# Kernel optimization log

Hardware: AMD Instinct MI355X
Metric: run time of the kernel (lower is better)

## Reference

```python
import jax, jax.numpy as jnp
import numpy as np

T, B, H, NH = 1024, 4, 1024, 16
D = H // NH


def setup_inputs() -> dict:
    key = jax.random.key(0)
    ks = jax.random.split(key, 8)
    s = 0.02
    return {
        "x": jax.random.normal(ks[0], (T, B, H), jnp.float32),
        "pos": jax.random.normal(ks[1], (2 * T - 1, 1, H), jnp.float32),
        "attn_mask": jnp.zeros((T, T), jnp.bool_),
        "ln_w": jnp.ones((H,), jnp.float32),
        "ln_b": jnp.zeros((H,), jnp.float32),
        "in_proj_w": jax.random.normal(ks[2], (3 * H, H), jnp.float32) * s,
        "in_proj_b": jnp.zeros((3 * H,), jnp.float32),
        "pos_proj_w": jax.random.normal(ks[3], (H, H), jnp.float32) * s,
        "r_w_bias": jax.random.normal(ks[4], (NH, D), jnp.float32) * s,
        "r_r_bias": jax.random.normal(ks[5], (NH, D), jnp.float32) * s,
        "out_proj_w": jax.random.normal(ks[6], (H, H), jnp.float32) * s,
        "out_proj_b": jnp.zeros((H,), jnp.float32),
    }


def _layer_norm(x, w, b, eps=1e-5):
    m = jnp.mean(x, axis=-1, keepdims=True)
    v = jnp.var(x, axis=-1, keepdims=True)
    return (x - m) * jax.lax.rsqrt(v + eps) * w + b


def _rel_shift(x):
    # x: [qlen, 2*qlen-1, B, NH] -> Transformer-XL relative shift
    q = x.shape[0]
    zero_pad = jnp.zeros((q, 1) + x.shape[2:], x.dtype)
    xp = jnp.concatenate([zero_pad, x], axis=1)            # [q, 2q, B, NH]
    xp = xp.reshape((x.shape[1] + 1, q) + x.shape[2:])     # [2q, q, B, NH]
    return xp[1:].reshape(x.shape)                         # [q, 2q-1, B, NH]


def reference(x, pos, attn_mask, ln_w, ln_b, in_proj_w, in_proj_b,
              pos_proj_w, r_w_bias, r_r_bias, out_proj_w, out_proj_b):
    # pre-norm
    qn = _layer_norm(x, ln_w, ln_b)                        # [T,B,H]
    # fused qkv projection
    qkv = qn @ in_proj_w.T + in_proj_b                     # [T,B,3H]
    q, k, v = jnp.split(qkv, 3, axis=-1)
    q = q.reshape(T, B, NH, D)
    k = k.reshape(T, B, NH, D)
    v = v.reshape(T, B, NH, D)
    # relative position keys (bias-free projection)
    r = (pos[:, 0] @ pos_proj_w.T).reshape(2 * T - 1, NH, D)
    # content term (AC) and position term (BD), Transformer-XL style
    AC = jnp.einsum('ibnd,jbnd->ijbn', q + r_w_bias, k)    # [T,T,B,NH]
    BD = jnp.einsum('ibnd,jnd->ijbn', q + r_r_bias, r)     # [T,2T-1,B,NH]
    BD = _rel_shift(BD)[:, :T]                             # [T,T,B,NH]
    scale = 1.0 / np.sqrt(D).astype(np.float32)
    score = (AC + BD) * scale
    score = jnp.where(attn_mask[:, :, None, None], -jnp.inf, score)
    p = jax.nn.softmax(score, axis=1)                      # coverage
    out = jnp.einsum('ijbn,jbnd->ibnd', p, v).reshape(T, B, H)
    o = out @ out_proj_w.T + out_proj_b                    # residual dropout = identity (eval)
    return o
```

## Files before the change

kernel.cpp:

```cpp
#include <hip/hip_runtime.h>
#include <hip/hip_bf16.h>
#include <math.h>

#define T_DIM 1024
#define B_DIM 4
#define H_DIM 1024
#define NHEAD 16
#define DHEAD 64
#define NROWS (T_DIM * B_DIM)
#define LPOS  (2 * T_DIM - 1)
#define QS    (3 * H_DIM)

typedef __attribute__((ext_vector_type(8))) short bfrag;
typedef __attribute__((ext_vector_type(4))) short sh4;
typedef __attribute__((ext_vector_type(4))) float facc;

static __device__ __forceinline__ short f2bf(float f) {
    return __builtin_bit_cast(short, __float2bfloat16(f));
}
static __device__ __forceinline__ float bf2f(short s) {
    unsigned u = ((unsigned)(unsigned short)s) << 16;
    return __builtin_bit_cast(float, u);
}

#define GLD16(g, l) __builtin_amdgcn_global_load_lds( \
    (const __attribute__((address_space(1))) void*)(g), \
    (__attribute__((address_space(3))) void*)(l), 16, 0, 0)

__global__ __launch_bounds__(256) void prep_kernel(
    const float* __restrict__ x, const float* __restrict__ lnw,
    const float* __restrict__ lnb, short* __restrict__ qn,
    const float* __restrict__ s0, short* __restrict__ d0, int c0,
    const float* __restrict__ s1, short* __restrict__ d1, int c1,
    const float* __restrict__ s2, short* __restrict__ d2, int c2,
    const float* __restrict__ s3, short* __restrict__ d3, int c3) {
    __shared__ float red0[4], red1[4];
    const int bid = blockIdx.x;
    const int tid = threadIdx.x;
    if (bid < NROWS) {
        const float* xr = x + (size_t)bid * H_DIM;
        short* yr = qn + (size_t)bid * H_DIM;
        float4 v = reinterpret_cast<const float4*>(xr)[tid];
        float s  = v.x + v.y + v.z + v.w;
        float sq = v.x * v.x + v.y * v.y + v.z * v.z + v.w * v.w;
        #pragma unroll
        for (int m = 32; m; m >>= 1) {
            s  += __shfl_xor(s, m);
            sq += __shfl_xor(sq, m);
        }
        int wave = tid >> 6, lane = tid & 63;
        if (lane == 0) { red0[wave] = s; red1[wave] = sq; }
        __syncthreads();
        float tot   = red0[0] + red0[1] + red0[2] + red0[3];
        float totsq = red1[0] + red1[1] + red1[2] + red1[3];
        float mean = tot * (1.0f / H_DIM);
        float var  = totsq * (1.0f / H_DIM) - mean * mean;
        float rstd = rsqrtf(var + 1e-5f);
        float4 wv = reinterpret_cast<const float4*>(lnw)[tid];
        float4 bv = reinterpret_cast<const float4*>(lnb)[tid];
        sh4 o;
        o[0] = f2bf((v.x - mean) * rstd * wv.x + bv.x);
        o[1] = f2bf((v.y - mean) * rstd * wv.y + bv.y);
        o[2] = f2bf((v.z - mean) * rstd * wv.z + bv.z);
        o[3] = f2bf((v.w - mean) * rstd * wv.w + bv.w);
        reinterpret_cast<sh4*>(yr)[tid] = o;
    } else {
        int i = (bid - NROWS) * 256 + tid;
        const float* s; short* d; int off;
        if      (i < c0)                { s = s0; d = d0; off = i; }
        else if (i < c0 + c1)           { s = s1; d = d1; off = i - c0; }
        else if (i < c0 + c1 + c2)      { s = s2; d = d2; off = i - c0 - c1; }
        else if (i < c0 + c1 + c2 + c3) { s = s3; d = d3; off = i - c0 - c1 - c2; }
        else return;
        const float* sp = s + (size_t)off * 8;
        float4 a = *(const float4*)(sp);
        float4 b = *(const float4*)(sp + 4);
        bfrag f;
        f[0] = f2bf(a.x); f[1] = f2bf(a.y); f[2] = f2bf(a.z); f[3] = f2bf(a.w);
        f[4] = f2bf(b.x); f[5] = f2bf(b.y); f[6] = f2bf(b.z); f[7] = f2bf(b.w);
        *(bfrag*)(d + (size_t)off * 8) = f;
    }
}

template<int MODE>
static __device__ __forceinline__ void gemm_body(
    const short* __restrict__ A, const short* __restrict__ B,
    const float* __restrict__ bias, void* __restrict__ Cv,
    int M, int N, int K, int gx, int nblk, int bid,
    short (*As)[64], short (*Bs)[64]) {
    const int tid = threadIdx.x;
    const int w4 = tid >> 6, l = tid & 63;
    const int lc = l & 15, lg = l >> 4;
    const int wr = w4 >> 1, wc = w4 & 1;

    const int cpx = nblk >> 3;
    const int nl = (bid & 7) * cpx + (bid >> 3);
    const int row0 = (nl / gx) * 128, col0 = (nl % gx) * 128;

    const int srow = l >> 3;
    const int schunk = ((l & 7) ^ srow) * 8;
    const int Mm1 = M - 1;

    facc acc[4][4];
    #pragma unroll
    for (int i = 0; i < 4; ++i)
        #pragma unroll
        for (int j = 0; j < 4; ++j) acc[i][j] = (facc){0.f, 0.f, 0.f, 0.f};

    for (int k0 = 0; k0 < K; k0 += 64) {
        #pragma unroll
        for (int p = 0; p < 4; ++p) {
            int rA = p * 32 + w4 * 8 + srow;
            int ga = row0 + rA; if (ga > Mm1) ga = Mm1;
            GLD16(A + (size_t)ga * K + k0 + schunk,
                  (char*)As + p * 4096 + w4 * 1024);
            GLD16(B + (size_t)(col0 + rA) * K + k0 + schunk,
                  (char*)Bs + p * 4096 + w4 * 1024);
        }
        __syncthreads();

        bfrag af[4][2], bfr[4][2];
        #pragma unroll
        for (int fr = 0; fr < 4; ++fr) {
            const int ra = wr * 64 + fr * 16 + lc;
            #pragma unroll
            for (int ks = 0; ks < 2; ++ks)
                af[fr][ks] = *(const bfrag*)&As[ra][(((ks * 4 + lg) ^ (ra & 7)) << 3)];
        }
        #pragma unroll
        for (int fc = 0; fc < 4; ++fc) {
            const int rb = wc * 64 + fc * 16 + lc;
            #pragma unroll
            for (int ks = 0; ks < 2; ++ks)
                bfr[fc][ks] = *(const bfrag*)&Bs[rb][(((ks * 4 + lg) ^ (rb & 7)) << 3)];
        }
        #pragma unroll
        for (int fr = 0; fr < 4; ++fr)
            #pragma unroll
            for (int fc = 0; fc < 4; ++fc)
                #pragma unroll
                for (int ks = 0; ks < 2; ++ks)
                    acc[fr][fc] = __builtin_amdgcn_mfma_f32_16x16x32_bf16(
                        af[fr][ks], bfr[fc][ks], acc[fr][fc], 0, 0, 0);
        __syncthreads();
    }

    #pragma unroll
    for (int fc = 0; fc < 4; ++fc) {
        const int gc = col0 + wc * 64 + fc * 16 + lc;
        const float bv = bias ? bias[gc] : 0.f;
        #pragma unroll
        for (int fr = 0; fr < 4; ++fr) {
            #pragma unroll
            for (int rg = 0; rg < 4; ++rg) {
                const int gr = row0 + wr * 64 + fr * 16 + lg * 4 + rg;
                if (gr < M) {
                    float o = acc[fr][fc][rg] + bv;
                    if constexpr (MODE == 0) ((float*)Cv)[(size_t)gr * N + gc] = o;
                    else                     ((short*)Cv)[(size_t)gr * N + gc] = f2bf(o);
                }
            }
        }
    }
}

__global__ __launch_bounds__(256) void gemm_dual(
    const short* __restrict__ A0, const short* __restrict__ B0,
    const float* __restrict__ bias0, short* __restrict__ C0,
    const short* __restrict__ A1, const short* __restrict__ B1,
    short* __restrict__ C1) {
    __shared__ short As[128][64];
    __shared__ short Bs[128][64];
    const int bid = blockIdx.x;
    if (bid < 768)
        gemm_body<1>(A0, B0, bias0, C0, NROWS, QS, H_DIM, QS / 128, 768, bid, As, Bs);
    else
        gemm_body<1>(A1, B1, nullptr, C1, LPOS, H_DIM, H_DIM, H_DIM / 128, 128, bid - 768, As, Bs);
}

__global__ __launch_bounds__(256) void gemm_f32out(
    const short* __restrict__ A, const short* __restrict__ B,
    const float* __restrict__ bias, float* __restrict__ C) {
    __shared__ short As[128][64];
    __shared__ short Bs[128][64];
    gemm_body<0>(A, B, bias, C, NROWS, H_DIM, H_DIM, H_DIM / 128, 256, blockIdx.x, As, Bs);
}

__global__ __launch_bounds__(256) void vtrans_kernel(const short* __restrict__ qkv,
                                                     short* __restrict__ vT) {
    __shared__ short T[64][72];
    const int tt = blockIdx.x, hh = blockIdx.y, b = blockIdx.z;
    const int tid = threadIdx.x;
    const int w = tid >> 6, lane = tid & 63;

    const int tg = tt * 64 + lane;
    const short* src = qkv + (size_t)(tg * B_DIM + b) * QS + 2 * H_DIM + hh * 64 + w * 16;
    bfrag v0 = *(const bfrag*)(src);
    bfrag v1 = *(const bfrag*)(src + 8);
    #pragma unroll
    for (int e = 0; e < 8; ++e) T[w * 16 + e][lane] = v0[e];
    #pragma unroll
    for (int e = 0; e < 8; ++e) T[w * 16 + 8 + e][lane] = v1[e];
    __syncthreads();

    const int hd = tid >> 2, tc = tid & 3;
    bfrag o0 = *(const bfrag*)&T[hd][tc * 16];
    bfrag o1 = *(const bfrag*)&T[hd][tc * 16 + 8];
    short* dst = vT + (((size_t)(b * H_DIM + hh * 64 + hd)) << 10) + tt * 64 + tc * 16;
    *(bfrag*)(dst) = o0;
    *(bfrag*)(dst + 8) = o1;
}

__global__ __launch_bounds__(512, 4) void attn_mfma(const short* __restrict__ qkv,
                                                    const short* __restrict__ r,
                                                    const short* __restrict__ vt,
                                                    const float* __restrict__ rwb,
                                                    const float* __restrict__ rrb,
                                                    short* __restrict__ out) {
    __shared__ short Ks[64][64];
    __shared__ short Vt[64][64];
    __shared__ short Rs[192][64];
    __shared__ short BDPs[8][16][84];

    const int d_   = blockIdx.x;
    const int slot = d_ >> 3, xcd = d_ & 7;
    const int bn   = xcd + 8 * (slot >> 3);
    const int i0   = (slot & 7) * 128;
    const int b    = bn >> 4;
    const int n    = bn & 15;

    const int tid = threadIdx.x;
    const int w   = tid >> 6;
    const int l   = tid & 63;
    const int lg  = l >> 4;
    const int lc  = l & 15;
    const int hoff = n * DHEAD;

    const int srow8 = l >> 3;
    const int sc8   = ((l & 7) ^ srow8) * 8;

    bfrag qw[2], qr[2];
    {
        const int row = i0 + 16 * w + lc;
        const short* qrow = qkv + (size_t)(row * B_DIM + b) * QS + hoff;
        #pragma unroll
        for (int ks = 0; ks < 2; ++ks) {
            const int d0 = ks * 32 + lg * 8;
            bfrag qv = *(const bfrag*)(qrow + d0);
            float4 wa = *(const float4*)(rwb + hoff + d0);
            float4 wb = *(const float4*)(rwb + hoff + d0 + 4);
            float4 ra = *(const float4*)(rrb + hoff + d0);
            float4 rb = *(const float4*)(rrb + hoff + d0 + 4);
            const float sc = 0.125f * 1.44269504f;
            float wf[8] = {wa.x, wa.y, wa.z, wa.w, wb.x, wb.y, wb.z, wb.w};
            float rf[8] = {ra.x, ra.y, ra.z, ra.w, rb.x, rb.y, rb.z, rb.w};
            bfrag fw, fr;
            #pragma unroll
            for (int e = 0; e < 8; ++e) {
                float qf = bf2f(qv[e]);
                fw[e] = f2bf((qf + wf[e]) * sc);
                fr[e] = f2bf((qf + rf[e]) * sc);
            }
            qw[ks] = fw; qr[ks] = fr;
        }
    }

    facc ofr[4];
    #pragma unroll
    for (int d = 0; d < 4; ++d) ofr[d] = (facc){0.f, 0.f, 0.f, 0.f};
    float lrow[4] = {0.f, 0.f, 0.f, 0.f};
    const int wbase = 16 * (7 - w);

    const short* kp = qkv + ((size_t)(w * 8 + srow8) * B_DIM + b) * QS + H_DIM + hoff + sc8;
    const short* vp = vt + (((size_t)(b * H_DIM + hoff + w * 8 + srow8)) << 10) + sc8;
    const size_t kstep = (size_t)64 * B_DIM * QS;
    bfrag* const ksd = (bfrag*)((char*)Ks + w * 1024 + l * 16);
    bfrag* const vtd = (bfrag*)((char*)Vt + w * 1024 + l * 16);

    bfrag stK, stV, stR[3];

    auto load_regs = [&](int jt) {
        const int l_min = jt * 64 + 896 - i0;
        stK = *(const bfrag*)(kp + (size_t)jt * kstep);
        stV = *(const bfrag*)(vp + jt * 64);
        #pragma unroll
        for (int p = 0; p < 3; ++p) {
            const int rr = (w * 3 + p) * 8 + srow8;
            int lrw = l_min + rr; if (lrw > 2046) lrw = 2046;
            stR[p] = *(const bfrag*)(r + (size_t)lrw * H_DIM + hoff + sc8);
        }
    };
    auto write_lds = [&]() {
        *ksd = stK;
        *vtd = stV;
        #pragma unroll
        for (int p = 0; p < 3; ++p)
            *(bfrag*)((char*)Rs + (w * 3 + p) * 1024 + l * 16) = stR[p];
    };

    load_regs(0);
    write_lds();
    __syncthreads();

    for (int jt = 0; jt < 16; ++jt) {
        if (jt < 15) load_regs(jt + 1);

        __builtin_amdgcn_s_setprio(1);
        facc sfr[4];
        #pragma unroll
        for (int js = 0; js < 4; ++js) {
            sfr[js] = (facc){-4.f, -4.f, -4.f, -4.f};
            const int jrow = js * 16 + lc;
            #pragma unroll
            for (int ks = 0; ks < 2; ++ks) {
                const int ch = (ks * 4 + lg) ^ (jrow & 7);
                bfrag bf = *(const bfrag*)&Ks[jrow][ch << 3];
                sfr[js] = __builtin_amdgcn_mfma_f32_16x16x32_bf16(qw[ks], bf, sfr[js], 0, 0, 0);
            }
        }
        #pragma unroll
        for (int ls = 0; ls < 5; ++ls) {
            facc bd = (facc){-4.f, -4.f, -4.f, -4.f};
            const int rrow = wbase + ls * 16 + lc;
            #pragma unroll
            for (int ks = 0; ks < 2; ++ks) {
                const int ch = (ks * 4 + lg) ^ (rrow & 7);
                bfrag bf = *(const bfrag*)&Rs[rrow][ch << 3];
                bd = __builtin_amdgcn_mfma_f32_16x16x32_bf16(qr[ks], bf, bd, 0, 0, 0);
            }
            #pragma unroll
            for (int rg = 0; rg < 4; ++rg)
                BDPs[w][lg * 4 + rg][ls * 16 + lc] = f2bf(bd[rg]);
        }
        __builtin_amdgcn_s_setprio(0);

        #pragma unroll
        for (int js = 0; js < 4; ++js)
            #pragma unroll
            for (int rg = 0; rg < 4; ++rg) {
                const int irow = lg * 4 + rg;
                float v = sfr[js][rg] + bf2f(BDPs[w][irow][js * 16 + lc - irow + 15]);
                float p = exp2f(v);
                lrow[rg] += p;
                BDPs[w][irow][js * 16 + lc] = f2bf(p);
            }

        bfrag pf[2];
        #pragma unroll
        for (int ks = 0; ks < 2; ++ks)
            pf[ks] = *(const bfrag*)&BDPs[w][lc][ks * 32 + lg * 8];
        __builtin_amdgcn_s_setprio(1);
        #pragma unroll
        for (int d = 0; d < 4; ++d) {
            #pragma unroll
            for (int ks = 0; ks < 2; ++ks) {
                const int vr = d * 16 + lc;
                const int ch = (ks * 4 + lg) ^ (vr & 7);
                bfrag vf = *(const bfrag*)&Vt[vr][ch << 3];
                ofr[d] = __builtin_amdgcn_mfma_f32_16x16x32_bf16(pf[ks], vf, ofr[d], 0, 0, 0);
            }
        }
        __builtin_amdgcn_s_setprio(0);

        __syncthreads();
        if (jt < 15) {
            write_lds();
            __syncthreads();
        }
    }

    #pragma unroll
    for (int m = 1; m < 16; m <<= 1)
        #pragma unroll
        for (int rg = 0; rg < 4; ++rg)
            lrow[rg] += __shfl_xor(lrow[rg], m);

    #pragma unroll
    for (int rg = 0; rg < 4; ++rg) {
        const float inv = 1.0f / lrow[rg];
        const int row = i0 + 16 * w + lg * 4 + rg;
        short* orow = out + (size_t)(row * B_DIM + b) * H_DIM + hoff;
        #pragma unroll
        for (int d = 0; d < 4; ++d)
            orow[d * 16 + lc] = f2bf(ofr[d][rg] * inv);
    }
}

extern "C" void kernel_launch(void* const* d_in, const int* in_sizes, int n_in,
                              void* d_out, int out_size, void* d_ws, size_t ws_size,
                              hipStream_t stream) {
    const float* x          = (const float*)d_in[0];
    const float* pos        = (const float*)d_in[1];
    const float* ln_w       = (const float*)d_in[3];
    const float* ln_b       = (const float*)d_in[4];
    const float* in_proj_w  = (const float*)d_in[5];
    const float* in_proj_b  = (const float*)d_in[6];
    const float* pos_proj_w = (const float*)d_in[7];
    const float* r_w_bias   = (const float*)d_in[8];
    const float* r_r_bias   = (const float*)d_in[9];
    const float* out_proj_w = (const float*)d_in[10];
    const float* out_proj_b = (const float*)d_in[11];
    float* out = (float*)d_out;

    short* qn   = (short*)d_ws;
    short* qkv  = qn + (size_t)NROWS * H_DIM;
    short* rbuf = qkv + (size_t)NROWS * QS;
    short* wi   = rbuf + (size_t)2048 * H_DIM;
    short* wp   = wi + (size_t)QS * H_DIM;
    short* wo   = wp + (size_t)H_DIM * H_DIM;
    short* posb = wo + (size_t)H_DIM * H_DIM;
    short* vT   = posb + (size_t)2048 * H_DIM;

    const int c0 = (LPOS * H_DIM) / 8;
    const int c1 = (QS * H_DIM) / 8;
    const int c2 = (H_DIM * H_DIM) / 8;
    const int c3 = c2;
    const int nchunk = c0 + c1 + c2 + c3;
    const int cvtblk = (nchunk + 255) / 256;
    prep_kernel<<<NROWS + cvtblk, 256, 0, stream>>>(
        x, ln_w, ln_b, qn,
        pos, posb, c0, in_proj_w, wi, c1, pos_proj_w, wp, c2, out_proj_w, wo, c3);

    gemm_dual<<<768 + 128, 256, 0, stream>>>(qn, wi, in_proj_b, qkv, posb, wp, rbuf);

    vtrans_kernel<<<dim3(16, 16, 4), 256, 0, stream>>>(qkv, vT);

    attn_mfma<<<512, 512, 0, stream>>>(
        qkv, rbuf, vT, r_w_bias, r_r_bias, qn);

    gemm_f32out<<<256, 256, 0, stream>>>(qn, wo, out_proj_b, out);
}
```

Measured before the change: 165.1 us.

## Keep relative-position window in an LDS ring buffer across key tiles

Each key tile needs a 192-row window of the projected position matrix R, and consecutive windows overlap by 128 rows. Instead of reloading and rewriting all 192 rows every iteration, the LDS R buffer becomes a ring indexed with a rotating offset, and each iteration fetches and stores only the 64 new rows. This cuts global R loads and LDS stores per iteration by about three times and lowers staging register use. The cost is a little extra index arithmetic on every R read in the BD MFMA loop.

```diff
diff --git a/kernel.cpp b/kernel.cpp
--- a/kernel.cpp
+++ b/kernel.cpp
@@ -270,6 +270,7 @@
     for (int d = 0; d < 4; ++d) ofr[d] = (facc){0.f, 0.f, 0.f, 0.f};
     float lrow[4] = {0.f, 0.f, 0.f, 0.f};
     const int wbase = 16 * (7 - w);
+    const int base0 = 896 - i0;
 
     const short* kp = qkv + ((size_t)(w * 8 + srow8) * B_DIM + b) * QS + H_DIM + hoff + sc8;
     const short* vp = vt + (((size_t)(b * H_DIM + hoff + w * 8 + srow8)) << 10) + sc8;
@@ -277,33 +278,36 @@
     bfrag* const ksd = (bfrag*)((char*)Ks + w * 1024 + l * 16);
     bfrag* const vtd = (bfrag*)((char*)Vt + w * 1024 + l * 16);
 
-    bfrag stK, stV, stR[3];
-
-    auto load_regs = [&](int jt) {
-        const int l_min = jt * 64 + 896 - i0;
-        stK = *(const bfrag*)(kp + (size_t)jt * kstep);
-        stV = *(const bfrag*)(vp + jt * 64);
+    bfrag stK, stV, stR;
+
+    {
+        stK = *(const bfrag*)(kp);
+        stV = *(const bfrag*)(vp);
+        bfrag r3[3];
         #pragma unroll
         for (int p = 0; p < 3; ++p) {
-            const int rr = (w * 3 + p) * 8 + srow8;
-            int lrw = l_min + rr; if (lrw > 2046) lrw = 2046;
-            stR[p] = *(const bfrag*)(r + (size_t)lrw * H_DIM + hoff + sc8);
-        }
-    };
-    auto write_lds = [&]() {
+            int lrw = base0 + (w * 3 + p) * 8 + srow8;
+            if (lrw > 2046) lrw = 2046;
+            r3[p] = *(const bfrag*)(r + (size_t)lrw * H_DIM + hoff + sc8);
+        }
         *ksd = stK;
         *vtd = stV;
         #pragma unroll
         for (int p = 0; p < 3; ++p)
-            *(bfrag*)((char*)Rs + (w * 3 + p) * 1024 + l * 16) = stR[p];
-    };
-
-    load_regs(0);
-    write_lds();
+            *(bfrag*)((char*)Rs + (w * 3 + p) * 1024 + l * 16) = r3[p];
+    }
     __syncthreads();
 
+    int off = 0;
+
     for (int jt = 0; jt < 16; ++jt) {
-        if (jt < 15) load_regs(jt + 1);
+        if (jt < 15) {
+            stK = *(const bfrag*)(kp + (size_t)(jt + 1) * kstep);
+            stV = *(const bfrag*)(vp + (jt + 1) * 64);
+            int lrw = base0 + jt * 64 + 192 + w * 8 + srow8;
+            if (lrw > 2046) lrw = 2046;
+            stR = *(const bfrag*)(r + (size_t)lrw * H_DIM + hoff + sc8);
+        }
 
         __builtin_amdgcn_s_setprio(1);
         facc sfr[4];
@@ -322,10 +326,11 @@
         for (int ls = 0; ls < 5; ++ls) {
             facc bd = (facc){-4.f, -4.f, -4.f, -4.f};
             const int rrow = wbase + ls * 16 + lc;
+            int pr = rrow + off; if (pr >= 192) pr -= 192;
             #pragma unroll
             for (int ks = 0; ks < 2; ++ks) {
                 const int ch = (ks * 4 + lg) ^ (rrow & 7);
-                bfrag bf = *(const bfrag*)&Rs[rrow][ch << 3];
+                bfrag bf = *(const bfrag*)&Rs[pr][ch << 3];
                 bd = __builtin_amdgcn_mfma_f32_16x16x32_bf16(qr[ks], bf, bd, 0, 0, 0);
             }
             #pragma unroll
@@ -364,8 +369,11 @@
 
         __syncthreads();
         if (jt < 15) {
-            write_lds();
+            *ksd = stK;
+            *vtd = stV;
+            *(bfrag*)((char*)Rs + ((off >> 3) + w) * 1024 + l * 16) = stR;
             __syncthreads();
+            off += 64; if (off == 192) off = 0;
         }
     }
 
```

Result: faster. 161.0 us (-2.5%).
